# Kernel optimization log

Hardware: AMD Instinct MI355X
Metric: run time of the kernel (lower is better)

## Reference

```python
import jax, jax.numpy as jnp
import numpy as np
from jax import lax

B, H, W = 512, 128, 128
ARCH = [1, 4096, 4096, 4096, 4096]
CONV_THRESH = 0.0
GRAPH_THRESH = 0.8
EMBED_DIM = 1


def setup_inputs() -> dict:
    key = jax.random.key(0)
    ks = jax.random.split(key, 16)
    inp = {
        "x": jax.random.normal(ks[0], (B, 1, H, W), dtype=jnp.float32),
        "conv_w": jax.random.normal(ks[1], (1, 1, 2, 2), dtype=jnp.float32) * 0.5,
        "conv_b": jax.random.normal(ks[2], (1,), dtype=jnp.float32) * 0.1,
        "rotation": jax.random.normal(ks[3], (EMBED_DIM, EMBED_DIM), dtype=jnp.float32),
        "entangle": jax.random.normal(ks[4], (EMBED_DIM, EMBED_DIM), dtype=jnp.float32),
    }
    # Linear params, torch convention W: [out_f, in_f]
    for i, (fi, fo) in enumerate(zip(ARCH[:-1], ARCH[1:])):
        inp[f"W{i+1}"] = jax.random.normal(ks[5 + 2 * i], (fo, fi), dtype=jnp.float32) / np.sqrt(fi)
        inp[f"b{i+1}"] = jax.random.normal(ks[6 + 2 * i], (fo,), dtype=jnp.float32) * 0.01
    return inp


def _forward(x, conv_w, conv_b, rotation, entangle, W1, b1, W2, b2, W3, b3, W4, b4):
    # ConvFilter: 2x2 valid conv, sigmoid(logits - thresh), mean over C,H,W -> [B]
    logits = lax.conv_general_dilated(
        x, conv_w, window_strides=(1, 1), padding="VALID",
        dimension_numbers=("NCHW", "OIHW", "NCHW"))
    logits = logits + conv_b.reshape(1, -1, 1, 1)
    conv_out = jax.nn.sigmoid(logits - CONV_THRESH).mean(axis=(1, 2, 3))  # [B]
    conv_vec = conv_out[:, None]  # [B, 1] -> embed_dim forced to 1

    # ClassicalSelfAttention (embed_dim = 1)
    q = conv_vec @ rotation                      # [B, 1]
    k = conv_vec @ entangle                      # [B, 1]
    scores = jax.nn.softmax((q @ k.T) / np.sqrt(EMBED_DIM).astype(np.float32), axis=-1)  # [B, B]
    attn_out = scores @ conv_vec                 # [B, 1]

    # tanh MLP stack
    out = attn_out
    acts = []
    for Wl, bl in ((W1, b1), (W2, b2), (W3, b3), (W4, b4)):
        out = jnp.tanh(out @ Wl.T + bl)          # [B, out_f]
        acts.append(out)

    # Vectorized fidelity adjacency over equal-shaped layer activations:
    # normalized Gram matrix squared, thresholded (replaces the O(L^2)
    # Python loop with .item() syncs in the source).
    S = jnp.stack([a.reshape(-1) for a in acts])                  # [L, B*4096]
    S_hat = S / (jnp.linalg.norm(S, axis=1, keepdims=True) + 1e-12)
    fid = (S_hat @ S_hat.T) ** 2                                   # [L, L]
    L = len(acts)
    weights = jnp.where(fid >= GRAPH_THRESH, 1.0, 0.0) * (1.0 - jnp.eye(L, dtype=fid.dtype))
    return out, weights


def reference(x, conv_w, conv_b, rotation, entangle, W1, b1, W2, b2, W3, b3, W4, b4):
    return _forward(x, conv_w, conv_b, rotation, entangle, W1, b1, W2, b2, W3, b3, W4, b4)
```

## Files before the change

kernel.cpp:

```cpp
#include <hip/hip_runtime.h>
#include <cmath>


#define NEL (512 * 4096)

typedef float  floatx4 __attribute__((ext_vector_type(4)));
typedef _Float16 halfx8 __attribute__((ext_vector_type(8)));
typedef _Float16 halfx4 __attribute__((ext_vector_type(4)));

#define BM 128
#define BN 128
#define BK 32
#define LDK 40

__global__ __launch_bounds__(256) void conv_mean_kernel(
    const float* __restrict__ x, const float* __restrict__ cw,
    const float* __restrict__ cb, float* __restrict__ c_out,
    float* __restrict__ D)
{
  __shared__ float sbuf[4];
  const int b = blockIdx.x;
  if (b == 0 && threadIdx.x < 160) D[threadIdx.x] = 0.f;
  const float w00 = cw[0], w01 = cw[1], w10 = cw[2], w11 = cw[3];
  const float bias = cb[0];
  const float* xb = x + (size_t)b * 128 * 128;
  float acc = 0.f;
  for (int t = threadIdx.x; t < 127 * 32; t += 256) {
    const int i  = t >> 5;
    const int j0 = (t & 31) << 2;
    const float* pr0 = xb + i * 128 + j0;
    const float* pr1 = pr0 + 128;
    const float4 a4 = *reinterpret_cast<const float4*>(pr0);
    const float  a5 = pr0[4];
    const float4 b4 = *reinterpret_cast<const float4*>(pr1);
    const float  b5 = pr1[4];
    const float a[5] = {a4.x, a4.y, a4.z, a4.w, a5};
    const float bb[5] = {b4.x, b4.y, b4.z, b4.w, b5};
    #pragma unroll
    for (int m = 0; m < 4; ++m) {
      if (j0 + m < 127) {
        float v = w00 * a[m] + w01 * a[m + 1] + w10 * bb[m] + w11 * bb[m + 1] + bias;
        acc += 1.0f / (1.0f + __expf(-v));
      }
    }
  }
  #pragma unroll
  for (int off = 32; off > 0; off >>= 1) acc += __shfl_down(acc, off, 64);
  const int lane = threadIdx.x & 63, wv = threadIdx.x >> 6;
  if (lane == 0) sbuf[wv] = acc;
  __syncthreads();
  if (threadIdx.x == 0)
    c_out[b] = (sbuf[0] + sbuf[1] + sbuf[2] + sbuf[3]) * (1.0f / 16129.0f);
}

__global__ __launch_bounds__(256) void attn_layer1_kernel(
    const float* __restrict__ c, const float* __restrict__ rot,
    const float* __restrict__ ent, const float* __restrict__ W1,
    const float* __restrict__ b1, float* __restrict__ act1,
    _Float16* __restrict__ a1h)
{
  __shared__ float sattn;
  const int i = blockIdx.x;
  if (threadIdx.x < 64) {
    const int lane = threadIdx.x;
    const float t = rot[0] * ent[0] * c[i];
    float vals[8], cj[8];
    float mx = -1e30f;
    #pragma unroll
    for (int u = 0; u < 8; ++u) {
      float cv = c[lane + u * 64];
      cj[u] = cv;
      vals[u] = t * cv;
      mx = fmaxf(mx, vals[u]);
    }
    #pragma unroll
    for (int off = 32; off > 0; off >>= 1) mx = fmaxf(mx, __shfl_down(mx, off, 64));
    mx = __shfl(mx, 0, 64);
    float se = 0.f, sw = 0.f;
    #pragma unroll
    for (int u = 0; u < 8; ++u) {
      float e = __expf(vals[u] - mx);
      se += e;
      sw += e * cj[u];
    }
    #pragma unroll
    for (int off = 32; off > 0; off >>= 1) {
      se += __shfl_down(se, off, 64);
      sw += __shfl_down(sw, off, 64);
    }
    if (lane == 0) sattn = sw / se;
  }
  __syncthreads();
  const float av = sattn;
  #pragma unroll
  for (int k = 0; k < 16; ++k) {
    const int o = k * 256 + threadIdx.x;
    const float v = tanhf(av * W1[o] + b1[o]);
    act1[(size_t)i * 4096 + o] = v;
    a1h[(size_t)i * 4096 + o] = (_Float16)v;
  }
}

__global__ __launch_bounds__(256) void wconv_kernel(
    const float* __restrict__ w, _Float16* __restrict__ wh)
{
  const int n8 = 4096 * 4096 / 8;
  const int stride = gridDim.x * 256;
  const float4* w4 = (const float4*)w;
  for (int i = blockIdx.x * 256 + threadIdx.x; i < n8; i += stride) {
    const float4 a = w4[2 * i];
    const float4 b = w4[2 * i + 1];
    halfx8 h = { (_Float16)a.x, (_Float16)a.y, (_Float16)a.z, (_Float16)a.w,
                 (_Float16)b.x, (_Float16)b.y, (_Float16)b.z, (_Float16)b.w };
    ((halfx8*)wh)[i] = h;
  }
}

__global__ __launch_bounds__(256, 4) void gemm_kernel(
    const _Float16* __restrict__ A16, const _Float16* __restrict__ W16,
    float* __restrict__ part)
{
  __shared__ _Float16 As[2][BM][LDK];
  __shared__ _Float16 Ws[2][BN][LDK];
  const int K = 4096, N = 4096;
  const int tid  = threadIdx.x;
  const int lane = tid & 63;
  const int wave = tid >> 6;
  const int wm = (wave >> 1) * 64;
  const int wn = (wave & 1) * 64;
  const int q  = lane >> 4;
  const int ml = lane & 15;
  const int tileM = blockIdx.y * BM;
  const int tileN = blockIdx.x * BN;
  const int Kslice = K / gridDim.z;
  const int kbeg = blockIdx.z * Kslice;
  const int kend = kbeg + Kslice;
  float* Cb = part + (size_t)blockIdx.z * NEL;

  floatx4 acc[4][4] = {};

  const int r0  = tid >> 2;
  const int cc0 = (tid & 3) << 3;

  halfx8 pa[2], pw[2];
  auto load_tile = [&](int k0) {
    #pragma unroll
    for (int u = 0; u < 2; ++u) {
      pa[u] = *reinterpret_cast<const halfx8*>(
          A16 + (size_t)(tileM + r0 + u * 64) * K + k0 + cc0);
      pw[u] = *reinterpret_cast<const halfx8*>(
          W16 + (size_t)(tileN + r0 + u * 64) * K + k0 + cc0);
    }
  };
  auto store_tile = [&](int buf) {
    #pragma unroll
    for (int u = 0; u < 2; ++u) {
      *reinterpret_cast<halfx8*>(&As[buf][r0 + u * 64][cc0]) = pa[u];
      *reinterpret_cast<halfx8*>(&Ws[buf][r0 + u * 64][cc0]) = pw[u];
    }
  };

  load_tile(kbeg);
  store_tile(0);
  int cur = 0;

  for (int k0 = kbeg; k0 < kend; k0 += BK) {
    const bool more = (k0 + BK < kend);
    if (more) load_tile(k0 + BK);

    asm volatile("s_waitcnt lgkmcnt(0)" ::: "memory");
    __builtin_amdgcn_s_barrier();

    halfx8 af[4], bf[4];
    #pragma unroll
    for (int i = 0; i < 4; ++i)
      af[i] = *reinterpret_cast<const halfx8*>(&As[cur][wm + i * 16 + ml][q * 8]);
    #pragma unroll
    for (int j = 0; j < 4; ++j)
      bf[j] = *reinterpret_cast<const halfx8*>(&Ws[cur][wn + j * 16 + ml][q * 8]);

    #pragma unroll
    for (int i = 0; i < 4; ++i)
      #pragma unroll
      for (int j = 0; j < 4; ++j)
        acc[i][j] = __builtin_amdgcn_mfma_f32_16x16x32_f16(af[i], bf[j], acc[i][j], 0, 0, 0);

    if (more) store_tile(cur ^ 1);
    cur ^= 1;
  }

  #pragma unroll
  for (int i = 0; i < 4; ++i) {
    const int row0 = tileM + wm + i * 16 + q * 4;
    #pragma unroll
    for (int j = 0; j < 4; ++j) {
      const int col = tileN + wn + j * 16 + ml;
      #pragma unroll
      for (int r = 0; r < 4; ++r)
        Cb[(size_t)(row0 + r) * N + col] = acc[i][j][r];
    }
  }
}

template<int S, bool H>
__global__ __launch_bounds__(256) void combine_tanh_kernel(
    const float* __restrict__ part, const float* __restrict__ bias,
    float* __restrict__ outp, _Float16* __restrict__ houtp)
{
  const int i4 = blockIdx.x * 256 + threadIdx.x;
  const floatx4* p4 = (const floatx4*)part;
  floatx4 s = p4[i4];
  #pragma unroll
  for (int z = 1; z < S; ++z) s += p4[(size_t)z * (NEL / 4) + i4];
  const floatx4 bv = ((const floatx4*)bias)[i4 & 1023];
  floatx4 o;
  #pragma unroll
  for (int r = 0; r < 4; ++r) o[r] = tanhf(s[r] + bv[r]);
  ((floatx4*)outp)[i4] = o;
  if (H) {
    halfx4 h = { (_Float16)o[0], (_Float16)o[1], (_Float16)o[2], (_Float16)o[3] };
    ((halfx4*)houtp)[i4] = h;
  }
}

__global__ __launch_bounds__(256) void fid_dots_kernel(
    const float* __restrict__ a1, const float* __restrict__ a2,
    const float* __restrict__ a3, const float* __restrict__ a4,
    float* __restrict__ D)
{
  __shared__ float sred[4][10];
  float s[10] = {0, 0, 0, 0, 0, 0, 0, 0, 0, 0};
  const int n4 = NEL / 4;
  const int stride = gridDim.x * blockDim.x;
  const floatx4* p1 = (const floatx4*)a1;
  const floatx4* p2 = (const floatx4*)a2;
  const floatx4* p3 = (const floatx4*)a3;
  const floatx4* p4 = (const floatx4*)a4;
  for (int i = blockIdx.x * 256 + threadIdx.x; i < n4; i += stride) {
    floatx4 v1 = p1[i], v2 = p2[i], v3 = p3[i], v4 = p4[i];
    #pragma unroll
    for (int r = 0; r < 4; ++r) {
      s[0] += v1[r] * v1[r]; s[1] += v1[r] * v2[r]; s[2] += v1[r] * v3[r];
      s[3] += v1[r] * v4[r]; s[4] += v2[r] * v2[r]; s[5] += v2[r] * v3[r];
      s[6] += v2[r] * v4[r]; s[7] += v3[r] * v3[r]; s[8] += v3[r] * v4[r];
      s[9] += v4[r] * v4[r];
    }
  }
  const int lane = threadIdx.x & 63, wv = threadIdx.x >> 6;
  #pragma unroll
  for (int p = 0; p < 10; ++p) {
    float v = s[p];
    #pragma unroll
    for (int off = 32; off > 0; off >>= 1) v += __shfl_down(v, off, 64);
    if (lane == 0) sred[wv][p] = v;
  }
  __syncthreads();
  if (threadIdx.x < 10) {
    float v = sred[0][threadIdx.x] + sred[1][threadIdx.x] +
              sred[2][threadIdx.x] + sred[3][threadIdx.x];
    atomicAdd(&D[threadIdx.x * 16], v);
  }
}

__global__ void finalize_kernel(const float* __restrict__ D, float* __restrict__ wout)
{
  const int i = threadIdx.x;
  if (i >= 16) return;
  const int p = i >> 2, qq = i & 3;
  const int a = p < qq ? p : qq;
  const int b = p < qq ? qq : p;
  const int base[4] = {0, 4, 7, 9};
  const float dpq = D[(base[a] + (b - a)) * 16];
  const float npv = sqrtf(D[base[p] * 16]) + 1e-12f;
  const float nqv = sqrtf(D[base[qq] * 16]) + 1e-12f;
  const float ch = dpq / (npv * nqv);
  const float fid = ch * ch;
  wout[i] = (fid >= 0.8f && p != qq) ? 1.0f : 0.0f;
}

extern "C" void kernel_launch(void* const* d_in, const int* in_sizes, int n_in,
                              void* d_out, int out_size, void* d_ws, size_t ws_size,
                              hipStream_t stream)
{
  const float* x   = (const float*)d_in[0];
  const float* cw  = (const float*)d_in[1];
  const float* cb  = (const float*)d_in[2];
  const float* rot = (const float*)d_in[3];
  const float* ent = (const float*)d_in[4];
  const float* W1  = (const float*)d_in[5];
  const float* b1  = (const float*)d_in[6];
  const float* W2  = (const float*)d_in[7];
  const float* b2  = (const float*)d_in[8];
  const float* W3  = (const float*)d_in[9];
  const float* b3  = (const float*)d_in[10];
  const float* W4  = (const float*)d_in[11];
  const float* b4  = (const float*)d_in[12];
  float* out = (float*)d_out;

  char*  ws    = (char*)d_ws;
  float* c_buf = (float*)(ws + 0);
  float* D     = (float*)(ws + 4096);
  float* act1  = (float*)(ws + 8192);
  float* act2  = act1 + NEL;
  float* act3  = act2 + NEL;
  _Float16* a1h = (_Float16*)(act3 + NEL);
  _Float16* a2h = a1h + NEL;
  _Float16* a3h = a2h + NEL;
  _Float16* wh  = a3h + NEL;
  float* part  = (float*)(wh + (size_t)4096 * 4096);
  float* wout  = out + NEL;

  const size_t base_need = 8192 + (size_t)3 * NEL * 4 + (size_t)3 * NEL * 2
                         + (size_t)4096 * 4096 * 2;
  const bool sk8 = ws_size >= base_need + (size_t)8 * NEL * 4;

  conv_mean_kernel<<<512, 256, 0, stream>>>(x, cw, cb, c_buf, D);
  attn_layer1_kernel<<<512, 256, 0, stream>>>(c_buf, rot, ent, W1, b1, act1, a1h);

  const int cgrid = NEL / 4 / 256;
  if (sk8) {
    dim3 g(32, 4, 8);
    wconv_kernel<<<2048, 256, 0, stream>>>(W2, wh);
    gemm_kernel<<<g, 256, 0, stream>>>(a1h, wh, part);
    combine_tanh_kernel<8, true><<<cgrid, 256, 0, stream>>>(part, b2, act2, a2h);
    wconv_kernel<<<2048, 256, 0, stream>>>(W3, wh);
    gemm_kernel<<<g, 256, 0, stream>>>(a2h, wh, part);
    combine_tanh_kernel<8, true><<<cgrid, 256, 0, stream>>>(part, b3, act3, a3h);
    wconv_kernel<<<2048, 256, 0, stream>>>(W4, wh);
    gemm_kernel<<<g, 256, 0, stream>>>(a3h, wh, part);
    combine_tanh_kernel<8, false><<<cgrid, 256, 0, stream>>>(part, b4, out, nullptr);
  } else {
    dim3 g(32, 4, 4);
    wconv_kernel<<<2048, 256, 0, stream>>>(W2, wh);
    gemm_kernel<<<g, 256, 0, stream>>>(a1h, wh, part);
    combine_tanh_kernel<4, true><<<cgrid, 256, 0, stream>>>(part, b2, act2, a2h);
    wconv_kernel<<<2048, 256, 0, stream>>>(W3, wh);
    gemm_kernel<<<g, 256, 0, stream>>>(a2h, wh, part);
    combine_tanh_kernel<4, true><<<cgrid, 256, 0, stream>>>(part, b3, act3, a3h);
    wconv_kernel<<<2048, 256, 0, stream>>>(W4, wh);
    gemm_kernel<<<g, 256, 0, stream>>>(a3h, wh, part);
    combine_tanh_kernel<4, false><<<cgrid, 256, 0, stream>>>(part, b4, out, nullptr);
  }

  fid_dots_kernel<<<256, 256, 0, stream>>>(act1, act2, act3, out, D);
  finalize_kernel<<<1, 64, 0, stream>>>(D, wout);
}
```

Baseline: 404.1 us.

## Fuse weight conversion into neighbor kernels and fold fidelity dots into final combine

Weight fp32->fp16 conversion for the next layer now runs in extra blocks appended to the preceding attention/combine kernels, so it overlaps with that work instead of being a separate launch. The last combine kernel also computes the ten fidelity dot products from its fresh outputs, and the final block finalizes the adjacency using a last-block atomic counter. This removes the standalone fid_dots and finalize passes, including re-reading the final activation, and cuts launch count. The cost is per-block atomics (2048 atomic adds per dot term instead of 256) and a last-block finalize pattern that relies on the D counter being zeroed, which is why the zeroing range grows to 168.

```diff
diff --git a/kernel.cpp b/kernel.cpp
--- a/kernel.cpp
+++ b/kernel.cpp
@@ -20,7 +20,7 @@
 {
   __shared__ float sbuf[4];
   const int b = blockIdx.x;
-  if (b == 0 && threadIdx.x < 160) D[threadIdx.x] = 0.f;
+  if (b == 0 && threadIdx.x < 168) D[threadIdx.x] = 0.f;
   const float w00 = cw[0], w01 = cw[1], w10 = cw[2], w11 = cw[3];
   const float bias = cb[0];
   const float* xb = x + (size_t)b * 128 * 128;
@@ -53,12 +53,32 @@
     c_out[b] = (sbuf[0] + sbuf[1] + sbuf[2] + sbuf[3]) * (1.0f / 16129.0f);
 }
 
-__global__ __launch_bounds__(256) void attn_layer1_kernel(
+__device__ __forceinline__ void wconv_body(const float* __restrict__ w,
+                                           _Float16* __restrict__ wh,
+                                           int start, int stride)
+{
+  const int n8 = 4096 * 4096 / 8;
+  const float4* w4 = (const float4*)w;
+  for (int i = start; i < n8; i += stride) {
+    const float4 a = w4[2 * i];
+    const float4 b = w4[2 * i + 1];
+    halfx8 h = { (_Float16)a.x, (_Float16)a.y, (_Float16)a.z, (_Float16)a.w,
+                 (_Float16)b.x, (_Float16)b.y, (_Float16)b.z, (_Float16)b.w };
+    ((halfx8*)wh)[i] = h;
+  }
+}
+
+__global__ __launch_bounds__(256) void attn_l1w_kernel(
     const float* __restrict__ c, const float* __restrict__ rot,
     const float* __restrict__ ent, const float* __restrict__ W1,
     const float* __restrict__ b1, float* __restrict__ act1,
-    _Float16* __restrict__ a1h)
-{
+    _Float16* __restrict__ a1h,
+    const float* __restrict__ wsrc, _Float16* __restrict__ wdst)
+{
+  if (blockIdx.x >= 512) {
+    wconv_body(wsrc, wdst, (blockIdx.x - 512) * 256 + threadIdx.x, 2048 * 256);
+    return;
+  }
   __shared__ float sattn;
   const int i = blockIdx.x;
   if (threadIdx.x < 64) {
@@ -98,21 +118,6 @@
     const float v = tanhf(av * W1[o] + b1[o]);
     act1[(size_t)i * 4096 + o] = v;
     a1h[(size_t)i * 4096 + o] = (_Float16)v;
-  }
-}
-
-__global__ __launch_bounds__(256) void wconv_kernel(
-    const float* __restrict__ w, _Float16* __restrict__ wh)
-{
-  const int n8 = 4096 * 4096 / 8;
-  const int stride = gridDim.x * 256;
-  const float4* w4 = (const float4*)w;
-  for (int i = blockIdx.x * 256 + threadIdx.x; i < n8; i += stride) {
-    const float4 a = w4[2 * i];
-    const float4 b = w4[2 * i + 1];
-    halfx8 h = { (_Float16)a.x, (_Float16)a.y, (_Float16)a.z, (_Float16)a.w,
-                 (_Float16)b.x, (_Float16)b.y, (_Float16)b.z, (_Float16)b.w };
-    ((halfx8*)wh)[i] = h;
   }
 }
 
@@ -202,11 +207,16 @@
   }
 }
 
-template<int S, bool H>
-__global__ __launch_bounds__(256) void combine_tanh_kernel(
+template<int S>
+__global__ __launch_bounds__(256) void combine_w_kernel(
     const float* __restrict__ part, const float* __restrict__ bias,
-    float* __restrict__ outp, _Float16* __restrict__ houtp)
-{
+    float* __restrict__ outp, _Float16* __restrict__ houtp,
+    const float* __restrict__ wsrc, _Float16* __restrict__ wdst)
+{
+  if (blockIdx.x >= 2048) {
+    wconv_body(wsrc, wdst, (blockIdx.x - 2048) * 256 + threadIdx.x, 2048 * 256);
+    return;
+  }
   const int i4 = blockIdx.x * 256 + threadIdx.x;
   const floatx4* p4 = (const floatx4*)part;
   floatx4 s = p4[i4];
@@ -217,39 +227,46 @@
   #pragma unroll
   for (int r = 0; r < 4; ++r) o[r] = tanhf(s[r] + bv[r]);
   ((floatx4*)outp)[i4] = o;
-  if (H) {
-    halfx4 h = { (_Float16)o[0], (_Float16)o[1], (_Float16)o[2], (_Float16)o[3] };
-    ((halfx4*)houtp)[i4] = h;
-  }
-}
-
-__global__ __launch_bounds__(256) void fid_dots_kernel(
+  halfx4 h = { (_Float16)o[0], (_Float16)o[1], (_Float16)o[2], (_Float16)o[3] };
+  ((halfx4*)houtp)[i4] = h;
+}
+
+template<int S>
+__global__ __launch_bounds__(256) void combine_fid_kernel(
+    const float* __restrict__ part, const float* __restrict__ bias,
+    float* __restrict__ outp,
     const float* __restrict__ a1, const float* __restrict__ a2,
-    const float* __restrict__ a3, const float* __restrict__ a4,
-    float* __restrict__ D)
+    const float* __restrict__ a3, float* __restrict__ D,
+    float* __restrict__ wout)
 {
   __shared__ float sred[4][10];
-  float s[10] = {0, 0, 0, 0, 0, 0, 0, 0, 0, 0};
-  const int n4 = NEL / 4;
-  const int stride = gridDim.x * blockDim.x;
-  const floatx4* p1 = (const floatx4*)a1;
-  const floatx4* p2 = (const floatx4*)a2;
-  const floatx4* p3 = (const floatx4*)a3;
-  const floatx4* p4 = (const floatx4*)a4;
-  for (int i = blockIdx.x * 256 + threadIdx.x; i < n4; i += stride) {
-    floatx4 v1 = p1[i], v2 = p2[i], v3 = p3[i], v4 = p4[i];
-    #pragma unroll
-    for (int r = 0; r < 4; ++r) {
-      s[0] += v1[r] * v1[r]; s[1] += v1[r] * v2[r]; s[2] += v1[r] * v3[r];
-      s[3] += v1[r] * v4[r]; s[4] += v2[r] * v2[r]; s[5] += v2[r] * v3[r];
-      s[6] += v2[r] * v4[r]; s[7] += v3[r] * v3[r]; s[8] += v3[r] * v4[r];
-      s[9] += v4[r] * v4[r];
-    }
+  __shared__ int slast;
+  const int i4 = blockIdx.x * 256 + threadIdx.x;
+  const floatx4* p4 = (const floatx4*)part;
+  floatx4 s = p4[i4];
+  #pragma unroll
+  for (int z = 1; z < S; ++z) s += p4[(size_t)z * (NEL / 4) + i4];
+  const floatx4 bv = ((const floatx4*)bias)[i4 & 1023];
+  floatx4 o;
+  #pragma unroll
+  for (int r = 0; r < 4; ++r) o[r] = tanhf(s[r] + bv[r]);
+  ((floatx4*)outp)[i4] = o;
+
+  const floatx4 v1 = ((const floatx4*)a1)[i4];
+  const floatx4 v2 = ((const floatx4*)a2)[i4];
+  const floatx4 v3 = ((const floatx4*)a3)[i4];
+  float sc[10] = {0, 0, 0, 0, 0, 0, 0, 0, 0, 0};
+  #pragma unroll
+  for (int r = 0; r < 4; ++r) {
+    sc[0] += v1[r] * v1[r]; sc[1] += v1[r] * v2[r]; sc[2] += v1[r] * v3[r];
+    sc[3] += v1[r] * o[r];  sc[4] += v2[r] * v2[r]; sc[5] += v2[r] * v3[r];
+    sc[6] += v2[r] * o[r];  sc[7] += v3[r] * v3[r]; sc[8] += v3[r] * o[r];
+    sc[9] += o[r] * o[r];
   }
   const int lane = threadIdx.x & 63, wv = threadIdx.x >> 6;
   #pragma unroll
   for (int p = 0; p < 10; ++p) {
-    float v = s[p];
+    float v = sc[p];
     #pragma unroll
     for (int off = 32; off > 0; off >>= 1) v += __shfl_down(v, off, 64);
     if (lane == 0) sred[wv][p] = v;
@@ -260,22 +277,24 @@
               sred[2][threadIdx.x] + sred[3][threadIdx.x];
     atomicAdd(&D[threadIdx.x * 16], v);
   }
-}
-
-__global__ void finalize_kernel(const float* __restrict__ D, float* __restrict__ wout)
-{
-  const int i = threadIdx.x;
-  if (i >= 16) return;
-  const int p = i >> 2, qq = i & 3;
-  const int a = p < qq ? p : qq;
-  const int b = p < qq ? qq : p;
-  const int base[4] = {0, 4, 7, 9};
-  const float dpq = D[(base[a] + (b - a)) * 16];
-  const float npv = sqrtf(D[base[p] * 16]) + 1e-12f;
-  const float nqv = sqrtf(D[base[qq] * 16]) + 1e-12f;
-  const float ch = dpq / (npv * nqv);
-  const float fid = ch * ch;
-  wout[i] = (fid >= 0.8f && p != qq) ? 1.0f : 0.0f;
+  __threadfence();
+  __syncthreads();
+  if (threadIdx.x == 0)
+    slast = (atomicAdd((int*)&D[160], 1) == (int)gridDim.x - 1) ? 1 : 0;
+  __syncthreads();
+  if (slast && threadIdx.x < 16) {
+    const int i = threadIdx.x;
+    const int p = i >> 2, qq = i & 3;
+    const int a = p < qq ? p : qq;
+    const int b = p < qq ? qq : p;
+    const int base[4] = {0, 4, 7, 9};
+    const float dpq = atomicAdd(&D[(base[a] + (b - a)) * 16], 0.0f);
+    const float npv = sqrtf(atomicAdd(&D[base[p] * 16], 0.0f)) + 1e-12f;
+    const float nqv = sqrtf(atomicAdd(&D[base[qq] * 16], 0.0f)) + 1e-12f;
+    const float ch = dpq / (npv * nqv);
+    const float fid = ch * ch;
+    wout[i] = (fid >= 0.8f && p != qq) ? 1.0f : 0.0f;
+  }
 }
 
 extern "C" void kernel_launch(void* const* d_in, const int* in_sizes, int n_in,
@@ -315,33 +334,26 @@
   const bool sk8 = ws_size >= base_need + (size_t)8 * NEL * 4;
 
   conv_mean_kernel<<<512, 256, 0, stream>>>(x, cw, cb, c_buf, D);
-  attn_layer1_kernel<<<512, 256, 0, stream>>>(c_buf, rot, ent, W1, b1, act1, a1h);
-
-  const int cgrid = NEL / 4 / 256;
+  attn_l1w_kernel<<<2560, 256, 0, stream>>>(c_buf, rot, ent, W1, b1,
+                                            act1, a1h, W2, wh);
+
   if (sk8) {
     dim3 g(32, 4, 8);
-    wconv_kernel<<<2048, 256, 0, stream>>>(W2, wh);
     gemm_kernel<<<g, 256, 0, stream>>>(a1h, wh, part);
-    combine_tanh_kernel<8, true><<<cgrid, 256, 0, stream>>>(part, b2, act2, a2h);
-    wconv_kernel<<<2048, 256, 0, stream>>>(W3, wh);
+    combine_w_kernel<8><<<4096, 256, 0, stream>>>(part, b2, act2, a2h, W3, wh);
     gemm_kernel<<<g, 256, 0, stream>>>(a2h, wh, part);
-    combine_tanh_kernel<8, true><<<cgrid, 256, 0, stream>>>(part, b3, act3, a3h);
-    wconv_kernel<<<2048, 256, 0, stream>>>(W4, wh);
+    combine_w_kernel<8><<<4096, 256, 0, stream>>>(part, b3, act3, a3h, W4, wh);
     gemm_kernel<<<g, 256, 0, stream>>>(a3h, wh, part);
-    combine_tanh_kernel<8, false><<<cgrid, 256, 0, stream>>>(part, b4, out, nullptr);
+    combine_fid_kernel<8><<<2048, 256, 0, stream>>>(part, b4, out,
+                                                    act1, act2, act3, D, wout);
   } else {
     dim3 g(32, 4, 4);
-    wconv_kernel<<<2048, 256, 0, stream>>>(W2, wh);
     gemm_kernel<<<g, 256, 0, stream>>>(a1h, wh, part);
-    combine_tanh_kernel<4, true><<<cgrid, 256, 0, stream>>>(part, b2, act2, a2h);
-    wconv_kernel<<<2048, 256, 0, stream>>>(W3, wh);
+    combine_w_kernel<4><<<4096, 256, 0, stream>>>(part, b2, act2, a2h, W3, wh);
     gemm_kernel<<<g, 256, 0, stream>>>(a2h, wh, part);
-    combine_tanh_kernel<4, true><<<cgrid, 256, 0, stream>>>(part, b3, act3, a3h);
-    wconv_kernel<<<2048, 256, 0, stream>>>(W4, wh);
+    combine_w_kernel<4><<<4096, 256, 0, stream>>>(part, b3, act3, a3h, W4, wh);
     gemm_kernel<<<g, 256, 0, stream>>>(a3h, wh, part);
-    combine_tanh_kernel<4, false><<<cgrid, 256, 0, stream>>>(part, b4, out, nullptr);
-  }
-
-  fid_dots_kernel<<<256, 256, 0, stream>>>(act1, act2, act3, out, D);
-  finalize_kernel<<<1, 64, 0, stream>>>(D, wout);
-}
+    combine_fid_kernel<4><<<2048, 256, 0, stream>>>(part, b4, out,
+                                                    act1, act2, act3, D, wout);
+  }
+}
```

Result: slower. 590.0 us (+46.0%).
